# Optimization experiments

Hardware: AMD Instinct MI355X
Metric: run time of the kernel (lower is better)

## Reference

```python
import jax, jax.numpy as jnp
import numpy as np

B, S, D, H, L, E, F, K, V = 4, 1024, 768, 12, 2, 8, 3072, 2, 50257
HD = D // H
EPS = 1e-6
N_TIME, N_LOC, N_ROAD, N_WEATHER = 288, 1000, 10, 8


def rmsnorm(x, w):
    return x / jnp.sqrt(jnp.mean(x * x, axis=-1, keepdims=True) + EPS) * w


def rope_cache(seq_len, dim):
    inv_freq = 1.0 / (10000.0 ** (jnp.arange(0, dim, 2, dtype=jnp.float32) / dim))
    freqs = jnp.arange(seq_len, dtype=jnp.float32)[:, None] * inv_freq[None, :]
    emb = jnp.concatenate([freqs, freqs], axis=-1)  # [S, HD]
    return jnp.cos(emb), jnp.sin(emb)


def rotate_half(x):
    h = x.shape[-1] // 2
    return jnp.concatenate([-x[..., h:], x[..., :h]], axis=-1)


def attention(x, Wq, Wk, Wv, Wo, cos, sin):
    b, s, d = x.shape
    def heads(w):
        return (x @ w).reshape(b, s, H, HD).transpose(0, 2, 1, 3)  # [B,H,S,HD]
    q, k, v = heads(Wq), heads(Wk), heads(Wv)
    c, sn = cos[None, None], sin[None, None]
    q = q * c + rotate_half(q) * sn
    k = k * c + rotate_half(k) * sn
    scores = jnp.einsum('bhqd,bhkd->bhqk', q, k) / jnp.sqrt(jnp.float32(HD))
    mask = jnp.tril(jnp.ones((s, s), dtype=bool))
    scores = jnp.where(mask[None, None], scores, jnp.finfo(scores.dtype).min)
    probs = jax.nn.softmax(scores, axis=-1)
    out = jnp.einsum('bhqk,bhkd->bhqd', probs, v)
    return out.transpose(0, 2, 1, 3).reshape(b, s, d) @ Wo


def moe(x, router_w, Wg, Wu, Wd):
    # x: [T, D]; top-k routed SwiGLU experts, combine weights renormalized over top-k
    probs = jax.nn.softmax(x @ router_w, axis=-1)              # [T, E]
    w, idx = jax.lax.top_k(probs, K)                           # [T, K]
    w = w / jnp.sum(w, axis=-1, keepdims=True)
    onehot = jax.nn.one_hot(idx, E, dtype=x.dtype)             # [T, K, E]
    combine = jnp.sum(onehot * w[..., None], axis=1)           # [T, E]
    out = jnp.zeros_like(x)
    for e in range(E):  # small fixed expert count
        h = jax.nn.silu(x @ Wg[e]) * (x @ Wu[e])               # [T, F]
        out = out + combine[:, e, None] * (h @ Wd[e])
    usage = jnp.mean(jnp.sum(onehot, axis=1), axis=0)          # [E]
    aux = jnp.sum(usage * jnp.mean(probs, axis=0)) * E
    return out, aux


def setup_inputs() -> dict:
    key = jax.random.key(0)
    ks = jax.random.split(key, 40)
    p = lambda i, shape: 0.02 * jax.random.normal(ks[i], shape, dtype=jnp.float32)
    inp = {}
    inp['input_ids'] = jax.random.randint(ks[0], (B, S), 0, V)
    inp['time_slots'] = jax.random.randint(ks[1], (B, 1), 0, N_TIME)
    inp['day_of_week'] = jax.random.randint(ks[2], (B, 1), 0, 7)
    inp['month'] = jax.random.randint(ks[3], (B, 1), 0, 12)
    inp['is_holiday'] = jax.random.randint(ks[4], (B, 1), 0, 2)
    inp['location_ids'] = jax.random.randint(ks[5], (B, 1), 0, N_LOC)
    inp['road_types'] = jax.random.randint(ks[6], (B, 1), 0, N_ROAD)
    inp['weather_states'] = jax.random.randint(ks[7], (B, 1), 0, N_WEATHER)
    inp['word_emb'] = p(8, (V, D))
    inp['time_emb'] = p(9, (N_TIME, D // 4))
    inp['dow_emb'] = p(10, (7, D // 4))
    inp['month_emb'] = p(11, (12, D // 4))
    inp['hol_emb'] = p(12, (2, D // 4))
    inp['loc_emb'] = p(13, (N_LOC, D // 2))
    inp['road_emb'] = p(14, (N_ROAD, D // 4))
    inp['weather_emb'] = p(15, (N_WEATHER, D // 4))
    inp['proj_w'] = p(16, (3 * D, D))
    inp['proj_b'] = jnp.zeros((D,), dtype=jnp.float32)
    inp['emb_norm_w'] = jnp.ones((D,), dtype=jnp.float32)
    inp['norm1_w'] = jnp.ones((L, D), dtype=jnp.float32)
    inp['Wq'] = p(17, (L, D, D))
    inp['Wk'] = p(18, (L, D, D))
    inp['Wv'] = p(19, (L, D, D))
    inp['Wo'] = p(20, (L, D, D))
    inp['norm2_w'] = jnp.ones((L, D), dtype=jnp.float32)
    inp['router_w'] = p(21, (L, D, E))
    inp['Wg'] = p(22, (L, E, D, F))
    inp['Wu'] = p(23, (L, E, D, F))
    inp['Wd'] = p(24, (L, E, F, D))
    inp['final_norm_w'] = jnp.ones((D,), dtype=jnp.float32)
    return inp


def reference(input_ids, time_slots, day_of_week, month, is_holiday, location_ids,
              road_types, weather_states, word_emb, time_emb, dow_emb, month_emb,
              hol_emb, loc_emb, road_emb, weather_emb, proj_w, proj_b, emb_norm_w,
              norm1_w, Wq, Wk, Wv, Wo, norm2_w, router_w, Wg, Wu, Wd, final_norm_w):
    b, s = input_ids.shape
    we = word_emb[input_ids]                                                  # [B,S,D]
    te = jnp.concatenate([time_emb[time_slots], dow_emb[day_of_week],
                          month_emb[month], hol_emb[is_holiday]], axis=-1)    # [B,1,D]
    le = loc_emb[location_ids]                                                # [B,1,D/2]
    ce = jnp.concatenate([road_emb[road_types], weather_emb[weather_states]], axis=-1)
    te = jnp.broadcast_to(te, (b, s, D))
    le = jnp.broadcast_to(le, (b, s, D // 2))
    ce = jnp.broadcast_to(ce, (b, s, D // 2))
    x = jnp.concatenate([we, te, le, ce], axis=-1) @ proj_w + proj_b          # [B,S,D]
    x = rmsnorm(x, emb_norm_w)
    cos, sin = rope_cache(s, HD)
    aux_total = jnp.float32(0.0)
    for l in range(L):
        x = x + attention(rmsnorm(x, norm1_w[l]), Wq[l], Wk[l], Wv[l], Wo[l], cos, sin)
        m, aux = moe(rmsnorm(x, norm2_w[l]).reshape(b * s, D),
                     router_w[l], Wg[l], Wu[l], Wd[l])
        x = x + m.reshape(b, s, D)
        aux_total = aux_total + aux
    x = rmsnorm(x, final_norm_w)
    return x, aux_total
```

## Files before the change

kernel.cpp:

```cpp
#include <hip/hip_runtime.h>
#include <math.h>


#define TTOK 4096
#define FDIM 3072
#define MAXSLOT 9216

typedef __attribute__((ext_vector_type(8))) short short8;
typedef __attribute__((ext_vector_type(4))) float f32x4;

__device__ __forceinline__ float bf2f(unsigned short u) {
  return __uint_as_float(((unsigned int)u) << 16);
}
__device__ __forceinline__ unsigned short f2bf(float f) {
  unsigned int u = __float_as_uint(f);
  u += 0x7fffu + ((u >> 16) & 1u);
  return (unsigned short)(u >> 16);
}
__device__ __forceinline__ void split3f(float a, unsigned short& h, unsigned short& m,
                                        unsigned short& l) {
  h = f2bf(a);
  float r = a - bf2f(h);
  m = f2bf(r);
  r -= bf2f(m);
// ... 76 lines not shown
    dst[di] = h; dst[di + dPS] = m; dst[di + 2 * dPS] = lo;
  }
}

__global__ void tconv2_k(const float* __restrict__ src, unsigned short* __restrict__ dst,
                         size_t dPS, int K, int N, size_t sstride, size_t dstride) {
  __shared__ float tile[32][33];
  src += (size_t)blockIdx.z * sstride;
  size_t dbase = (size_t)blockIdx.z * dstride;
  int n0 = blockIdx.x * 32, k0 = blockIdx.y * 32;
  int tx = threadIdx.x, ty = threadIdx.y;
  #pragma unroll
  for (int r = 0; r < 4; ++r)
    tile[ty + r * 8][tx] = src[(size_t)(k0 + ty + r * 8) * N + n0 + tx];
  __syncthreads();
  #pragma unroll
  for (int r = 0; r < 4; ++r) {
    int n = n0 + ty + r * 8;
    unsigned short h, m;
    split2f(tile[tx][ty + r * 8], h, m);
    size_t di = dbase + (size_t)n * K + k0 + tx;
    dst[di] = h; dst[di + dPS] = m;
  }
}

__global__ void tconv_k(const float* __restrict__ src, unsigned short* __restrict__ dst,
                        int K, int N, size_t sstride, size_t dstride) {
  __shared__ unsigned short tile[32][33];
  src += (size_t)blockIdx.z * sstride;
  unsigned short* d = dst + (size_t)blockIdx.z * dstride;
  int n0 = blockIdx.x * 32, k0 = blockIdx.y * 32;
  int tx = threadIdx.x, ty = threadIdx.y;
  #pragma unroll
  for (int r = 0; r < 4; ++r)
    tile[ty + r * 8][tx] = f2bf(src[(size_t)(k0 + ty + r * 8) * N + n0 + tx]);
  __syncthreads();
  #pragma unroll
  for (int r = 0; r < 4; ++r) {
    int n = n0 + ty + r * 8;
    d[(size_t)n * K + k0 + tx] = tile[tx][ty + r * 8];
  }
}

__global__ void gconv3_k(const float* __restrict__ we, const int* __restrict__ ids,
                         unsigned short* __restrict__ x3, size_t pPS) {
  int t = blockIdx.x;
  int d = threadIdx.x << 2;
  float4 v = *(const float4*)(we + (size_t)ids[t] * 768 + d);
  ushort4 vh, vm, vl;
  split3f(v.x, vh.x, vm.x, vl.x);
  split3f(v.y, vh.y, vm.y, vl.y);
  split3f(v.z, vh.z, vm.z, vl.z);
  split3f(v.w, vh.w, vm.w, vl.w);
  size_t o = (size_t)t * 768 + d;
  *(ushort4*)(x3 + o) = vh;
  *(ushort4*)(x3 + pPS + o) = vm;
  *(ushort4*)(x3 + 2 * pPS + o) = vl;
}

template <int OUT>
__global__ __launch_bounds__(256) void rmsnorm_k(const float* __restrict__ xin,
                                                 const float* __restrict__ w,
                                                 float* __restrict__ yf,
                                                 unsigned short* __restrict__ yb, size_t pPS) {
  int t = blockIdx.x;
  int tid = threadIdx.x;
  const float* xr = xin + (size_t)t * 768;
  float v0 = xr[tid], v1 = xr[tid + 256], v2 = xr[tid + 512];
  float ss = v0 * v0 + v1 * v1 + v2 * v2;
  #pragma unroll
  for (int o = 32; o > 0; o >>= 1) ss += __shfl_xor(ss, o);
  __shared__ float wss[4];
  if ((tid & 63) == 0) wss[tid >> 6] = ss;
  __syncthreads();
  float tot = wss[0] + wss[1] + wss[2] + wss[3];
  float inv = 1.0f / sqrtf(tot / 768.0f + 1e-6f);
  float o0 = v0 * inv * w[tid], o1 = v1 * inv * w[tid + 256], o2 = v2 * inv * w[tid + 512];
  if (OUT != 1) {
    float* yr = yf + (size_t)t * 768;
    yr[tid] = o0; yr[tid + 256] = o1; yr[tid + 512] = o2;
  }
  if (OUT == 1 || OUT == 2) {
    unsigned short* yr = yb + (size_t)t * 768;
    unsigned short h, m, l;
    split3f(o0, h, m, l); yr[tid] = h;       yr[tid + pPS] = m;       yr[tid + 2 * pPS] = l;
    split3f(o1, h, m, l); yr[tid + 256] = h; yr[tid + 256 + pPS] = m; yr[tid + 256 + 2 * pPS] = l;
    split3f(o2, h, m, l); yr[tid + 512] = h; yr[tid + 512 + pPS] = m; yr[tid + 512 + 2 * pPS] = l;
  }
  if (OUT == 3) {
    unsigned short* yr = yb + (size_t)t * 768;
    yr[tid] = f2bf(o0); yr[tid + 256] = f2bf(o1); yr[tid + 512] = f2bf(o2);
  }
}

__global__ __launch_bounds__(256) void rope_apply_k(float* __restrict__ qkv,
                                                    const float* __restrict__ cosb,
                                                    const float* __restrict__ sinb) {
  int idx = blockIdx.x * 256 + threadIdx.x;
  int j = idx & 31;
  int hh = (idx >> 5) % 12;
  int t = idx / 384;
  int s = t & 1023;
  float c = cosb[s * 32 + j], sn = sinb[s * 32 + j];
  size_t base = (size_t)t * 2304 + hh * 64 + j;
  float q1 = qkv[base], q2 = qkv[base + 32];
  qkv[base]      = q1 * c - q2 * sn;
  qkv[base + 32] = q2 * c + q1 * sn;
  size_t kb = base + 768;
  float k1 = qkv[kb], k2 = qkv[kb + 32];
  qkv[kb]      = k1 * c - k2 * sn;
  qkv[kb + 32] = k2 * c + k1 * sn;
}

template <int EPI>
__global__ __launch_bounds__(256) void gemm3(const unsigned short* __restrict__ A, size_t aPS,
                                             const unsigned short* __restrict__ BT, size_t bPS,
                                             float* __restrict__ Cf, int N, int K,
                                             const float* __restrict__ rowBias) {
  __shared__ __align__(16) unsigned short As[3][4096];
  __shared__ __align__(16) unsigned short Bs[3][4096];
  int tid = threadIdx.x, w = tid >> 6, l = tid & 63, lr = l & 15, lg = l >> 4;
  int m0 = blockIdx.y * 128, n0 = blockIdx.x * 128;
  size_t aoff = (size_t)(m0 + 32 * w + lr) * K + lg * 8;
  size_t boff = (size_t)(n0 + 32 * w + lr) * K + lg * 8;
  size_t aoff1 = aoff + (size_t)16 * K, boff1 = boff + (size_t)16 * K;
  f32x4 acc[4][4];
  #pragma unroll
  for (int i = 0; i < 4; ++i)
    #pragma unroll
    for (int j = 0; j < 4; ++j) acc[i][j] = (f32x4){0.f, 0.f, 0.f, 0.f};
  int wr = w >> 1, wc = w & 1;
  for (int k0 = 0; k0 < K; k0 += 32) {
    #pragma unroll
    for (int p = 0; p < 3; ++p) {
      gload16(A + p * aPS + aoff + k0,  &As[p][1024 * w]);
      gload16(A + p * aPS + aoff1 + k0, &As[p][1024 * w + 512]);
      gload16(BT + p * bPS + boff + k0,  &Bs[p][1024 * w]);
      gload16(BT + p * bPS + boff1 + k0, &Bs[p][1024 * w + 512]);
    }
    __syncthreads();
    short8 af[3][4], bf[3][4];
    #pragma unroll
    for (int p = 0; p < 3; ++p)
      #pragma unroll
      for (int i = 0; i < 4; ++i) {
        af[p][i] = *(const short8*)(&As[p][(wr * 4 + i) * 512 + l * 8]);
        bf[p][i] = *(const short8*)(&Bs[p][(wc * 4 + i) * 512 + l * 8]);
      }
    MFMA_SPLIT3(acc)
    __syncthreads();
  }
  int colb = n0 + wc * 64 + lr;
  int rowb = m0 + wr * 64 + lg * 4;
  #pragma unroll
  for (int i = 0; i < 4; ++i)
    #pragma unroll
    for (int j = 0; j < 4; ++j) {
      int col = colb + j * 16;
      #pragma unroll
      for (int r = 0; r < 4; ++r) {
        int row = rowb + i * 16 + r;
        size_t idx = (size_t)row * N + col;
        float v = acc[i][j][r];
        if (EPI == 0)      Cf[idx] = v;
        else if (EPI == 2) Cf[idx] += v;
        else               Cf[idx] = v + rowBias[(row >> 10) * 768 + col];
      }
    }
}

template <int FUSE>
__global__ __launch_bounds__(256) void gemm2_gu(const unsigned short* __restrict__ X3, size_t xPS,
    const unsigned short* __restrict__ W2, size_t wPS, float* __restrict__ outb,
    const float* __restrict__ gin, const int* __restrict__ slot_token,
    const int* __restrict__ offs, const unsigned short* __restrict__ zp) {
  __shared__ __align__(16) unsigned short As[2][4096];
  __shared__ __align__(16) unsigned short Bs[2][4096];
  int sb = blockIdx.y * 128;
  if (sb >= offs[8]) return;
  int e = 0;
  #pragma unroll
  for (int i = 1; i < 8; ++i) if (sb >= offs[i]) e = i;
  int tid = threadIdx.x, w = tid >> 6, l = tid & 63, lr = l & 15, lg = l >> 4;
  int n0 = blockIdx.x * 128;
  const unsigned short* WE = W2 + (size_t)e * FDIM * 768;
  int t0 = slot_token[sb + 32 * w + lr];
  int t1 = slot_token[sb + 32 * w + 16 + lr];
  const unsigned short* a0[2];
  const unsigned short* a1[2];
  #pragma unroll
  for (int p = 0; p < 2; ++p) {
    a0[p] = (t0 < 0 ? zp : X3 + p * xPS + (size_t)t0 * 768) + lg * 8;
    a1[p] = (t1 < 0 ? zp : X3 + p * xPS + (size_t)t1 * 768) + lg * 8;
  }
  size_t boff = (size_t)(n0 + 32 * w + lr) * 768 + lg * 8;
  size_t boff1 = boff + (size_t)16 * 768;
  f32x4 acc[4][4];
  #pragma unroll
  for (int i = 0; i < 4; ++i)
    #pragma unroll
    for (int j = 0; j < 4; ++j) acc[i][j] = (f32x4){0.f, 0.f, 0.f, 0.f};
  int wr = w >> 1, wc = w & 1;
  for (int k0 = 0; k0 < 768; k0 += 32) {
    #pragma unroll
    for (int p = 0; p < 2; ++p) {
      gload16(a0[p] + k0, &As[p][1024 * w]);
      gload16(a1[p] + k0, &As[p][1024 * w + 512]);
      gload16(WE + p * wPS + boff + k0,  &Bs[p][1024 * w]);
      gload16(WE + p * wPS + boff1 + k0, &Bs[p][1024 * w + 512]);
    }
    __syncthreads();
    short8 af[2][4], bf[2][4];
    #pragma unroll
    for (int p = 0; p < 2; ++p)
      #pragma unroll
      for (int i = 0; i < 4; ++i) {
        af[p][i] = *(const short8*)(&As[p][(wr * 4 + i) * 512 + l * 8]);
        bf[p][i] = *(const short8*)(&Bs[p][(wc * 4 + i) * 512 + l * 8]);
      }
    MFMA_SPLIT2(acc)
    __syncthreads();
  }
  int colb = n0 + wc * 64 + lr;
  int rowb = sb + wr * 64 + lg * 4;
  #pragma unroll
  for (int i = 0; i < 4; ++i)
    #pragma unroll
    for (int j = 0; j < 4; ++j) {
      int col = colb + j * 16;
      #pragma unroll
      for (int r = 0; r < 4; ++r) {
        size_t idx = (size_t)(rowb + i * 16 + r) * FDIM + col;
        float v = acc[i][j][r];
        if (FUSE == 0) outb[idx] = v;
        else {
          float g = gin[idx];
          outb[idx] = g / (1.0f + expf(-g)) * v;
        }
      }
    }
}

__global__ __launch_bounds__(256) void gemm2_dn(const float* __restrict__ hbf,
    const unsigned short* __restrict__ W2, size_t wPS, float* __restrict__ ob,
    const int* __restrict__ offs) {
  __shared__ __align__(16) unsigned short As[2][4096];
  __shared__ __align__(16) unsigned short Bs[2][4096];
  int sb = blockIdx.y * 128;
  if (sb >= offs[8]) return;
  int e = 0;
  #pragma unroll
  for (int i = 1; i < 8; ++i) if (sb >= offs[i]) e = i;
  int tid = threadIdx.x, w = tid >> 6, l = tid & 63, lr = l & 15, lg = l >> 4;
  int n0 = blockIdx.x * 128;
  const unsigned short* WE = W2 + (size_t)e * 768 * FDIM;
  size_t boff = (size_t)(n0 + 32 * w + lr) * FDIM + lg * 8;
  size_t boff1 = boff + (size_t)16 * FDIM;
  const float* ha0 = hbf + (size_t)(sb + 32 * w + lr) * FDIM + lg * 8;
  const float* ha1 = ha0 + (size_t)16 * FDIM;
  f32x4 acc[4][4];
  #pragma unroll
  for (int i = 0; i < 4; ++i)
    #pragma unroll
    for (int j = 0; j < 4; ++j) acc[i][j] = (f32x4){0.f, 0.f, 0.f, 0.f};
  int wr = w >> 1, wc = w & 1;
  for (int k0 = 0; k0 < FDIM; k0 += 32) {
    #pragma unroll
    for (int p = 0; p < 2; ++p) {
      gload16(WE + p * wPS + boff + k0,  &Bs[p][1024 * w]);
      gload16(WE + p * wPS + boff1 + k0, &Bs[p][1024 * w + 512]);
    }
    {
      float4 v0 = *(const float4*)(ha0 + k0);
      float4 v1 = *(const float4*)(ha0 + k0 + 4);
      float va[8] = {v0.x, v0.y, v0.z, v0.w, v1.x, v1.y, v1.z, v1.w};
      short8 sh, sm;
      #pragma unroll
      for (int q = 0; q < 8; ++q) {
        unsigned short a, b;
        split2f(va[q], a, b);
        sh[q] = (short)a; sm[q] = (short)b;
      }
      *(short8*)(&As[0][1024 * w + l * 8]) = sh;
      *(short8*)(&As[1][1024 * w + l * 8]) = sm;
      v0 = *(const float4*)(ha1 + k0);
      v1 = *(const float4*)(ha1 + k0 + 4);
      float vb[8] = {v0.x, v0.y, v0.z, v0.w, v1.x, v1.y, v1.z, v1.w};
      #pragma unroll
      for (int q = 0; q < 8; ++q) {
        unsigned short a, b;
        split2f(vb[q], a, b);
        sh[q] = (short)a; sm[q] = (short)b;
      }
      *(short8*)(&As[0][1024 * w + 512 + l * 8]) = sh;
      *(short8*)(&As[1][1024 * w + 512 + l * 8]) = sm;
    }
    __syncthreads();
    short8 af[2][4], bf[2][4];
    #pragma unroll
    for (int p = 0; p < 2; ++p)
      #pragma unroll
      for (int i = 0; i < 4; ++i) {
        af[p][i] = *(const short8*)(&As[p][(wr * 4 + i) * 512 + l * 8]);
        bf[p][i] = *(const short8*)(&Bs[p][(wc * 4 + i) * 512 + l * 8]);
      }
    MFMA_SPLIT2(acc)
    __syncthreads();
  }
  int colb = n0 + wc * 64 + lr;
  int rowb = sb + wr * 64 + lg * 4;
  #pragma unroll
  for (int i = 0; i < 4; ++i)
    #pragma unroll
    for (int j = 0; j < 4; ++j) {
      int col = colb + j * 16;
      #pragma unroll
      for (int r = 0; r < 4; ++r)
        ob[(size_t)(rowb + i * 16 + r) * 768 + col] = acc[i][j][r];
    }
}


__global__ __launch_bounds__(256) void gemm_gu(const unsigned short* __restrict__ xnb,
    const unsigned short* __restrict__ wgT, const unsigned short* __restrict__ wuT,
    unsigned short* __restrict__ hb, const int* __restrict__ slot_token,
    const int* __restrict__ offs, const unsigned short* __restrict__ zp) {
  __shared__ __align__(16) unsigned short As[4096], Bg[4096], Bu[4096];
  int sb = blockIdx.y * 128;
  if (sb >= offs[8]) return;
  int e = 0;
  #pragma unroll
  for (int i = 1; i < 8; ++i) if (sb >= offs[i]) e = i;
  int tid = threadIdx.x, w = tid >> 6, l = tid & 63, lr = l & 15, lg = l >> 4;
  int n0 = blockIdx.x * 128;
  int t0 = slot_token[sb + 32 * w + lr];
  int t1 = slot_token[sb + 32 * w + 16 + lr];
  const unsigned short* ga0 = (t0 < 0 ? zp : xnb + (size_t)t0 * 768) + lg * 8;
  const unsigned short* ga1 = (t1 < 0 ? zp : xnb + (size_t)t1 * 768) + lg * 8;
  const unsigned short* WgE = wgT + (size_t)e * FDIM * 768;
  const unsigned short* WuE = wuT + (size_t)e * FDIM * 768;
  const unsigned short* gg0 = WgE + (size_t)(n0 + 32 * w + lr) * 768 + lg * 8;
  const unsigned short* gg1 = gg0 + 16 * 768;
  const unsigned short* gu0 = WuE + (size_t)(n0 + 32 * w + lr) * 768 + lg * 8;
  const unsigned short* gu1 = gu0 + 16 * 768;
  f32x4 ag[4][4], au[4][4];
  #pragma unroll
  for (int i = 0; i < 4; ++i)
    #pragma unroll
    for (int j = 0; j < 4; ++j) {
      ag[i][j] = (f32x4){0.f, 0.f, 0.f, 0.f};
      au[i][j] = (f32x4){0.f, 0.f, 0.f, 0.f};
    }
  int wr = w >> 1, wc = w & 1;
  for (int k0 = 0; k0 < 768; k0 += 32) {
    gload16(ga0 + k0, As + 1024 * w);
    gload16(ga1 + k0, As + 1024 * w + 512);
    gload16(gg0 + k0, Bg + 1024 * w);
    gload16(gg1 + k0, Bg + 1024 * w + 512);
    gload16(gu0 + k0, Bu + 1024 * w);
    gload16(gu1 + k0, Bu + 1024 * w + 512);
    __syncthreads();
    short8 af[4];
    #pragma unroll
    for (int i = 0; i < 4; ++i) af[i] = *(const short8*)(As + (wr * 4 + i) * 512 + l * 8);
    #pragma unroll
    for (int j = 0; j < 4; ++j) {
      short8 bg = *(const short8*)(Bg + (wc * 4 + j) * 512 + l * 8);
      short8 bu = *(const short8*)(Bu + (wc * 4 + j) * 512 + l * 8);
      #pragma unroll
      for (int i = 0; i < 4; ++i) {
        ag[i][j] = __builtin_amdgcn_mfma_f32_16x16x32_bf16(af[i], bg, ag[i][j], 0, 0, 0);
        au[i][j] = __builtin_amdgcn_mfma_f32_16x16x32_bf16(af[i], bu, au[i][j], 0, 0, 0);
      }
    }
    __syncthreads();
  }
  int colb = n0 + wc * 64 + lr;
  int rowb = sb + wr * 64 + lg * 4;
  #pragma unroll
  for (int i = 0; i < 4; ++i)
    #pragma unroll
    for (int j = 0; j < 4; ++j) {
      int col = colb + j * 16;
      #pragma unroll
      for (int r = 0; r < 4; ++r) {
        float g = ag[i][j][r], u = au[i][j][r];
        hb[(size_t)(rowb + i * 16 + r) * FDIM + col] = f2bf(g / (1.0f + expf(-g)) * u);
      }
    }
}

__global__ __launch_bounds__(256) void gemm_d(const unsigned short* __restrict__ hb,
    const unsigned short* __restrict__ wdT, unsigned short* __restrict__ ob,
    const int* __restrict__ offs) {
  __shared__ __align__(16) unsigned short As[4096], Bs[4096];
  int sb = blockIdx.y * 128;
  if (sb >= offs[8]) return;
  int e = 0;
  #pragma unroll
  for (int i = 1; i < 8; ++i) if (sb >= offs[i]) e = i;
  int tid = threadIdx.x, w = tid >> 6, l = tid & 63, lr = l & 15, lg = l >> 4;
  int n0 = blockIdx.x * 128;
  const unsigned short* ga0 = hb + (size_t)(sb + 32 * w + lr) * FDIM + lg * 8;
  const unsigned short* ga1 = ga0 + (size_t)16 * FDIM;
  const unsigned short* WdE = wdT + (size_t)e * 768 * FDIM;
  const unsigned short* gb0 = WdE + (size_t)(n0 + 32 * w + lr) * FDIM + lg * 8;
  const unsigned short* gb1 = gb0 + (size_t)16 * FDIM;
  f32x4 acc[4][4];
  #pragma unroll
  for (int i = 0; i < 4; ++i)
    #pragma unroll
    for (int j = 0; j < 4; ++j) acc[i][j] = (f32x4){0.f, 0.f, 0.f, 0.f};
  int wr = w >> 1, wc = w & 1;
  for (int k0 = 0; k0 < FDIM; k0 += 32) {
    gload16(ga0 + k0, As + 1024 * w);
    gload16(ga1 + k0, As + 1024 * w + 512);
    gload16(gb0 + k0, Bs + 1024 * w);
    gload16(gb1 + k0, Bs + 1024 * w + 512);
    __syncthreads();
    short8 af[4], bf[4];
    #pragma unroll
    for (int i = 0; i < 4; ++i) af[i] = *(const short8*)(As + (wr * 4 + i) * 512 + l * 8);
    #pragma unroll
    for (int j = 0; j < 4; ++j) bf[j] = *(const short8*)(Bs + (wc * 4 + j) * 512 + l * 8);
    #pragma unroll
    for (int i = 0; i < 4; ++i)
      #pragma unroll
      for (int j = 0; j < 4; ++j)
        acc[i][j] = __builtin_amdgcn_mfma_f32_16x16x32_bf16(af[i], bf[j], acc[i][j], 0, 0, 0);
    __syncthreads();
  }
  int colb = n0 + wc * 64 + lr;
  int rowb = sb + wr * 64 + lg * 4;
  #pragma unroll
  for (int i = 0; i < 4; ++i)
    #pragma unroll
    for (int j = 0; j < 4; ++j) {
      int col = colb + j * 16;
      #pragma unroll
      for (int r = 0; r < 4; ++r)
        ob[(size_t)(rowb + i * 16 + r) * 768 + col] = f2bf(acc[i][j][r]);
    }
}

__global__ __launch_bounds__(256) void attn_k(const float* __restrict__ qkv,
                                              unsigned short* __restrict__ ax3, size_t pPS) {
  int pr = blockIdx.x, h = blockIdx.y, b = blockIdx.z;
  int tid = threadIdx.x;
  int ty4 = (tid >> 4) << 2, tx4 = (tid & 15) << 2;
  __shared__ float qs[64][68];
  __shared__ float kps[64][68];
  __shared__ float vs[64][68];
  int lr = tid >> 2;
  int lc = (tid & 3) << 4;
  for (int half = 0; half < 2; ++half) {
    int qt = half ? (15 - pr) : pr;
    int q0 = qt << 6;
    size_t qbase = ((size_t)(b * 1024 + q0 + lr)) * 2304 + h * 64 + lc;
    #pragma unroll
    for (int i = 0; i < 4; ++i) {
      float4 v = *(const float4*)(qkv + qbase + 4 * i);
      qs[lc + 4 * i + 0][lr] = v.x;
      qs[lc + 4 * i + 1][lr] = v.y;
      qs[lc + 4 * i + 2][lr] = v.z;
      qs[lc + 4 * i + 3][lr] = v.w;
    }
    float acc[4][4];
    float m[4], l[4];
    #pragma unroll
    for (int i = 0; i < 4; ++i) {
      m[i] = -3.0e38f; l[i] = 0.0f;
      #pragma unroll
      for (int j = 0; j < 4; ++j) acc[i][j] = 0.0f;
    }
    for (int kt = 0; kt <= qt; ++kt) {
      int k0 = kt << 6;
      __syncthreads();
      size_t kb = ((size_t)(b * 1024 + k0 + lr)) * 2304 + 768 + h * 64 + lc;
      #pragma unroll
      for (int i = 0; i < 4; ++i) {
        float4 kv = *(const float4*)(qkv + kb + 4 * i);
        kps[lc + 4 * i + 0][lr] = kv.x;
        kps[lc + 4 * i + 1][lr] = kv.y;
        kps[lc + 4 * i + 2][lr] = kv.z;
        kps[lc + 4 * i + 3][lr] = kv.w;
        *(float4*)&vs[lr][lc + 4 * i] = *(const float4*)(qkv + kb + 768 + 4 * i);
      }
      __syncthreads();
      float s[4][4];
      #pragma unroll
      for (int i = 0; i < 4; ++i)
        #pragma unroll
        for (int j = 0; j < 4; ++j) s[i][j] = 0.0f;
      #pragma unroll 8
      for (int d = 0; d < 64; ++d) {
        float4 qv = *(const float4*)&qs[d][ty4];
        float4 kv = *(const float4*)&kps[d][tx4];
        float qa[4] = {qv.x, qv.y, qv.z, qv.w};
        float ka[4] = {kv.x, kv.y, kv.z, kv.w};
        #pragma unroll
        for (int i = 0; i < 4; ++i)
          #pragma unroll
          for (int j = 0; j < 4; ++j) s[i][j] += qa[i] * ka[j];
      }
      bool diag = (kt == qt);
      #pragma unroll
      for (int i = 0; i < 4; ++i) {
        #pragma unroll
        for (int j = 0; j < 4; ++j) {
          if (diag && (tx4 + j > ty4 + i)) s[i][j] = -1.0e30f;
          else s[i][j] *= 0.125f;
        }
        float mx = fmaxf(fmaxf(s[i][0], s[i][1]), fmaxf(s[i][2], s[i][3]));
        mx = fmaxf(mx, __shfl_xor(mx, 1));
        mx = fmaxf(mx, __shfl_xor(mx, 2));
        mx = fmaxf(mx, __shfl_xor(mx, 4));
        mx = fmaxf(mx, __shfl_xor(mx, 8));
        float mnew = fmaxf(m[i], mx);
        float c = expf(m[i] - mnew);
        float rs = 0.0f;
        #pragma unroll
        for (int j = 0; j < 4; ++j) { s[i][j] = expf(s[i][j] - mnew); rs += s[i][j]; }
        rs += __shfl_xor(rs, 1);
        rs += __shfl_xor(rs, 2);
        rs += __shfl_xor(rs, 4);
        rs += __shfl_xor(rs, 8);
        l[i] = l[i] * c + rs;
        m[i] = mnew;
        #pragma unroll
        for (int j = 0; j < 4; ++j) acc[i][j] *= c;
      }
      __syncthreads();
      #pragma unroll
      for (int i = 0; i < 4; ++i)
        *(float4*)&kps[ty4 + i][tx4] = make_float4(s[i][0], s[i][1], s[i][2], s[i][3]);
      __syncthreads();
      #pragma unroll 4
      for (int kk = 0; kk < 16; ++kk) {
        float4 v0 = *(const float4*)&vs[(kk << 2) + 0][tx4];
        float4 v1 = *(const float4*)&vs[(kk << 2) + 1][tx4];
        float4 v2 = *(const float4*)&vs[(kk << 2) + 2][tx4];
        float4 v3 = *(const float4*)&vs[(kk << 2) + 3][tx4];
        #pragma unroll
        for (int i = 0; i < 4; ++i) {
          float4 p4 = *(const float4*)&kps[ty4 + i][kk << 2];
          acc[i][0] += p4.x * v0.x + p4.y * v1.x + p4.z * v2.x + p4.w * v3.x;
          acc[i][1] += p4.x * v0.y + p4.y * v1.y + p4.z * v2.y + p4.w * v3.y;
          acc[i][2] += p4.x * v0.z + p4.y * v1.z + p4.z * v2.z + p4.w * v3.z;
          acc[i][3] += p4.x * v0.w + p4.y * v1.w + p4.z * v2.w + p4.w * v3.w;
        }
      }
    }
    __syncthreads();
    #pragma unroll
    for (int i = 0; i < 4; ++i) {
      float invl = 1.0f / l[i];
      size_t ob = ((size_t)(b * 1024 + q0 + ty4 + i)) * 768 + h * 64 + tx4;
      ushort4 vh, vm, vl;
      unsigned short a0, a1, a2;
      split3f(acc[i][0] * invl, a0, a1, a2); vh.x = a0; vm.x = a1; vl.x = a2;
      split3f(acc[i][1] * invl, a0, a1, a2); vh.y = a0; vm.y = a1; vl.y = a2;
      split3f(acc[i][2] * invl, a0, a1, a2); vh.z = a0; vm.z = a1; vl.z = a2;
      split3f(acc[i][3] * invl, a0, a1, a2); vh.w = a0; vm.w = a1; vl.w = a2;
      *(ushort4*)(ax3 + ob) = vh;
      *(ushort4*)(ax3 + pPS + ob) = vm;
      *(ushort4*)(ax3 + 2 * pPS + ob) = vl;
    }
  }
}

__global__ __launch_bounds__(256) void router_k(const float* __restrict__ xn,
                                                const float* __restrict__ rw,
                                                int* __restrict__ tk_idx, float* __restrict__ tk_w,
                                                int* __restrict__ cnt, float* __restrict__ psum) {
  __shared__ float bps[8];
  __shared__ int bcnt[8];
  int tid = threadIdx.x;
  if (tid < 8) { bps[tid] = 0.0f; bcnt[tid] = 0; }
  __syncthreads();
  int t = blockIdx.x * 4 + (tid >> 6);
  int lane = tid & 63;
  const float* xr = xn + (size_t)t * 768;
  float p[8] = {};
  for (int d = lane; d < 768; d += 64) {
    float xv = xr[d];
    const float* wr = rw + (size_t)d * 8;
    #pragma unroll
    for (int e = 0; e < 8; ++e) p[e] += xv * wr[e];
  }
  #pragma unroll
  for (int e = 0; e < 8; ++e) {
    float v = p[e];
    #pragma unroll
    for (int o = 32; o > 0; o >>= 1) v += __shfl_xor(v, o);
    p[e] = v;
  }
  if (lane == 0) {
    float mx = p[0];
    #pragma unroll
    for (int e = 1; e < 8; ++e) mx = fmaxf(mx, p[e]);
    float s = 0.0f;
    #pragma unroll
    for (int e = 0; e < 8; ++e) { p[e] = expf(p[e] - mx); s += p[e]; }
    float invs = 1.0f / s;
    #pragma unroll
    for (int e = 0; e < 8; ++e) p[e] *= invs;
    int i1 = 0; float v1 = p[0];
    #pragma unroll
    for (int e = 1; e < 8; ++e) if (p[e] > v1) { v1 = p[e]; i1 = e; }
    int i2 = (i1 == 0) ? 1 : 0; float v2 = p[i2];
    #pragma unroll
    for (int e = 0; e < 8; ++e) if (e != i1 && p[e] > v2) { v2 = p[e]; i2 = e; }
    float wsum = v1 + v2;
    tk_idx[t * 2] = i1; tk_idx[t * 2 + 1] = i2;
    tk_w[t * 2] = v1 / wsum; tk_w[t * 2 + 1] = v2 / wsum;
    atomicAdd(&bcnt[i1], 1); atomicAdd(&bcnt[i2], 1);
    #pragma unroll
    for (int e = 0; e < 8; ++e) atomicAdd(&bps[e], p[e]);
  }
  __syncthreads();
  if (tid < 8) {
    atomicAdd(&cnt[tid], bcnt[tid]);
    atomicAdd(&psum[tid], bps[tid]);
  }
}

__global__ void moe_offsets_k(const int* __restrict__ cnt, int* __restrict__ offs,
                              const float* __restrict__ psum, float* __restrict__ aux) {
  if (threadIdx.x == 0) {
    int o = 0; float a = 0.0f;
    for (int e = 0; e < 8; ++e) {
      offs[e] = o;
      o += (cnt[e] + 127) & ~127;
      a += ((float)cnt[e] / 4096.0f) * (psum[e] / 4096.0f);
    }
    offs[8] = o;
    aux[0] += a * 8.0f;
  }
}

__global__ void moe_fill_k(const int* __restrict__ tk_idx, const int* __restrict__ offs,
                           int* __restrict__ fill, int* __restrict__ slot_token,
                           int* __restrict__ tk_slot) {
  int i = blockIdx.x * 256 + threadIdx.x;
  int e = tk_idx[i];
  int pos = atomicAdd(&fill[e], 1);
  int slot = offs[e] + pos;
  slot_token[slot] = i >> 1;
  tk_slot[i] = slot;
}

template <int BF>
__global__ void moe_combine_k(float* __restrict__ x, const void* __restrict__ osv,
                              const int* __restrict__ tk_slot, const float* __restrict__ tk_w) {
  int t = blockIdx.x;
  int d = threadIdx.x << 2;
  int s0 = tk_slot[t * 2], s1 = tk_slot[t * 2 + 1];
  float w0 = tk_w[t * 2], w1 = tk_w[t * 2 + 1];
  float a0, a1, a2, a3, b0, b1, b2, b3;
  if (BF == 0) {
    const float* os = (const float*)osv;
    float4 a = *(const float4*)(os + (size_t)s0 * 768 + d);
    float4 b = *(const float4*)(os + (size_t)s1 * 768 + d);
    a0 = a.x; a1 = a.y; a2 = a.z; a3 = a.w;
    b0 = b.x; b1 = b.y; b2 = b.z; b3 = b.w;
  } else {
    const unsigned short* os = (const unsigned short*)osv;
    ushort4 a = *(const ushort4*)(os + (size_t)s0 * 768 + d);
    ushort4 b = *(const ushort4*)(os + (size_t)s1 * 768 + d);
    a0 = bf2f(a.x); a1 = bf2f(a.y); a2 = bf2f(a.z); a3 = bf2f(a.w);
    b0 = bf2f(b.x); b1 = bf2f(b.y); b2 = bf2f(b.z); b3 = bf2f(b.w);
  }
  float4 c = *(const float4*)(x + (size_t)t * 768 + d);
  c.x += w0 * a0 + w1 * b0;
  c.y += w0 * a1 + w1 * b1;
  c.z += w0 * a2 + w1 * b2;
  c.w += w0 * a3 + w1 * b3;
  *(float4*)(x + (size_t)t * 768 + d) = c;
}

__global__ void write_aux_k(const float* __restrict__ aux, float* __restrict__ out) {
  out[0] = aux[0];
}


extern "C" void kernel_launch(void* const* d_in, const int* in_sizes, int n_in,
                              void* d_out, int out_size, void* d_ws, size_t ws_size,
                              hipStream_t stream) {
  const int* input_ids      = (const int*)d_in[0];
  const int* time_slots     = (const int*)d_in[1];
  const int* day_of_week    = (const int*)d_in[2];
  const int* month          = (const int*)d_in[3];
  const int* is_holiday     = (const int*)d_in[4];
  const int* location_ids   = (const int*)d_in[5];
  const int* road_types     = (const int*)d_in[6];
  const int* weather_states = (const int*)d_in[7];
  const float* word_emb     = (const float*)d_in[8];
  const float* time_emb     = (const float*)d_in[9];
  const float* dow_emb      = (const float*)d_in[10];
  const float* month_emb    = (const float*)d_in[11];
  const float* hol_emb      = (const float*)d_in[12];
  const float* loc_emb      = (const float*)d_in[13];
  const float* road_emb     = (const float*)d_in[14];
  const float* weather_emb  = (const float*)d_in[15];
  const float* proj_w       = (const float*)d_in[16];
  const float* proj_b       = (const float*)d_in[17];
  const float* emb_norm_w   = (const float*)d_in[18];
  const float* norm1_w     = (const float*)d_in[19];
  const float* Wq           = (const float*)d_in[20];
  const float* Wk           = (const float*)d_in[21];
  const float* Wv           = (const float*)d_in[22];
  const float* Wo           = (const float*)d_in[23];
  const float* norm2_w      = (const float*)d_in[24];
  const float* router_w     = (const float*)d_in[25];
  const float* Wg           = (const float*)d_in[26];
  const float* Wu           = (const float*)d_in[27];
  const float* Wd           = (const float*)d_in[28];
  const float* final_norm_w = (const float*)d_in[29];
  float* out = (float*)d_out;

  const size_t TD = (size_t)TTOK * 768;
  const size_t REG = (size_t)MAXSLOT * FDIM * 4;
  char* base = (char*)d_ws;
  auto carve = [&](size_t bytes) { char* p = base; base += (bytes + 255) & ~(size_t)255; return p; };
  float* x    = (float*)carve(TD * 4);
  float* xn   = (float*)carve(TD * 4);
  float* cosb = (float*)carve(32768 * 4);
  float* sinb = (float*)carve(32768 * 4);
  float* ctx  = (float*)carve(4 * 1536 * 4);
  float* biasB= (float*)carve(4 * 768 * 4);
  float* tkw  = (float*)carve(8192 * 4);
  float* psum = (float*)carve(64);
  float* auxa = (float*)carve(64);
  int* cnt    = (int*)carve(64);
  int* fill   = (int*)carve(64);
  int* offs   = (int*)carve(64);
  int* tk_idx = (int*)carve(8192 * 4);
  int* tk_slot= (int*)carve(8192 * 4);
  int* slot_token = (int*)carve(MAXSLOT * 4);
  unsigned short* zp = (unsigned short*)carve(4096);
  unsigned short* xnb3 = (unsigned short*)carve(3 * TD * 2);
  char* QAH = carve(REG);
  char* GT  = carve(REG);
  char* Wr  = carve(REG);
  float* qkv = (float*)QAH;
  unsigned short* ax3 = (unsigned short*)(QAH + (size_t)TTOK * 2304 * 4);
  float* hbf = (float*)QAH;
  unsigned short* hb16 = (unsigned short*)QAH;
  float* gtmp = (float*)GT;
  float* obf = (float*)GT;
  unsigned short* ob16 = (unsigned short*)GT;
  unsigned short* wpl = (unsigned short*)Wr;

  const size_t PS_D = (size_t)768 * 768;
  const size_t PS_QKV = (size_t)2304 * 768;
  const size_t PS_E = (size_t)8 * FDIM * 768;

  hipMemsetAsync(auxa, 0, 64, stream);
  hipMemsetAsync(zp, 0, 4096, stream);
  rope_cache_k<<<dim3(1024), dim3(32), 0, stream>>>(cosb, sinb);
  build_ctx_k<<<dim3(4, 6), dim3(256), 0, stream>>>(time_slots, day_of_week, month, is_holiday,
      location_ids, road_types, weather_states, time_emb, dow_emb, month_emb, hol_emb,
      loc_emb, road_emb, weather_emb, ctx);
  build_bias_k<<<dim3(4, 3), dim3(256), 0, stream>>>(ctx, proj_w, proj_b, biasB);
  tconv3_k<<<dim3(24, 24, 1), dim3(32, 8), 0, stream>>>(proj_w, wpl, PS_D, 768, 768, 0, 0);
  gconv3_k<<<dim3(TTOK), dim3(192), 0, stream>>>(word_emb, input_ids, xnb3, TD);
  gemm3<3><<<dim3(6, 32), dim3(256), 0, stream>>>(xnb3, TD, wpl, PS_D, xn, 768, 768, biasB);
  rmsnorm_k<0><<<dim3(TTOK), dim3(256), 0, stream>>>(xn, emb_norm_w, x, nullptr, 0);

  for (int l = 0; l < 2; ++l) {
    const float* rw = router_w + (size_t)l * 768 * 8;
    tconv3_k<<<dim3(24, 24, 1), dim3(32, 8), 0, stream>>>(Wq + (size_t)l * PS_D, wpl, PS_QKV, 768, 768, 0, 0);
    tconv3_k<<<dim3(24, 24, 1), dim3(32, 8), 0, stream>>>(Wk + (size_t)l * PS_D, wpl + PS_D, PS_QKV, 768, 768, 0, 0);
    tconv3_k<<<dim3(24, 24, 1), dim3(32, 8), 0, stream>>>(Wv + (size_t)l * PS_D, wpl + 2 * PS_D, PS_QKV, 768, 768, 0, 0);
    rmsnorm_k<1><<<dim3(TTOK), dim3(256), 0, stream>>>(x, norm1_w + l * 768, nullptr, xnb3, TD);
    gemm3<0><<<dim3(18, 32), dim3(256), 0, stream>>>(xnb3, TD, wpl, PS_QKV, qkv, 2304, 768, nullptr);
    rope_apply_k<<<dim3(6144), dim3(256), 0, stream>>>(qkv, cosb, sinb);
    attn_k<<<dim3(8, 12, 4), dim3(256), 0, stream>>>(qkv, ax3, TD);
    tconv3_k<<<dim3(24, 24, 1), dim3(32, 8), 0, stream>>>(Wo + (size_t)l * PS_D, wpl, PS_D, 768, 768, 0, 0);
    gemm3<2><<<dim3(6, 32), dim3(256), 0, stream>>>(ax3, TD, wpl, PS_D, x, 768, 768, nullptr);

    if (l == 0)
      rmsnorm_k<2><<<dim3(TTOK), dim3(256), 0, stream>>>(x, norm2_w, xn, xnb3, TD);
    else
      rmsnorm_k<3><<<dim3(TTOK), dim3(256), 0, stream>>>(x, norm2_w + 768, xn, xnb3, TD);
    hipMemsetAsync(cnt, 0, 64, stream);
    hipMemsetAsync(fill, 0, 64, stream);
    hipMemsetAsync(psum, 0, 64, stream);
    hipMemsetAsync(slot_token, 0xFF, MAXSLOT * 4, stream);
    router_k<<<dim3(1024), dim3(256), 0, stream>>>(xn, rw, tk_idx, tkw, cnt, psum);
    moe_offsets_k<<<dim3(1), dim3(64), 0, stream>>>(cnt, offs, psum, auxa);
    moe_fill_k<<<dim3(32), dim3(256), 0, stream>>>(tk_idx, offs, fill, slot_token, tk_slot);
    if (l == 0) {
      tconv2_k<<<dim3(96, 24, 8), dim3(32, 8), 0, stream>>>(Wg, wpl, PS_E,
          768, FDIM, (size_t)768 * FDIM, (size_t)FDIM * 768);
      gemm2_gu<0><<<dim3(24, MAXSLOT / 128), dim3(256), 0, stream>>>(xnb3, TD, wpl, PS_E,
          gtmp, nullptr, slot_token, offs, zp);
      tconv2_k<<<dim3(96, 24, 8), dim3(32, 8), 0, stream>>>(Wu, wpl, PS_E,
          768, FDIM, (size_t)768 * FDIM, (size_t)FDIM * 768);
      gemm2_gu<1><<<dim3(24, MAXSLOT / 128), dim3(256), 0, stream>>>(xnb3, TD, wpl, PS_E,
          hbf, gtmp, slot_token, offs, zp);
      tconv2_k<<<dim3(24, 96, 8), dim3(32, 8), 0, stream>>>(Wd, wpl, PS_E,
          FDIM, 768, (size_t)FDIM * 768, (size_t)768 * FDIM);
      gemm2_dn<<<dim3(6, MAXSLOT / 128), dim3(256), 0, stream>>>(hbf, wpl, PS_E, obf, offs);
      moe_combine_k<0><<<dim3(TTOK), dim3(192), 0, stream>>>(x, obf, tk_slot, tkw);
    } else {
      const float* wg1 = Wg + (size_t)8 * 768 * FDIM;
      const float* wu1 = Wu + (size_t)8 * 768 * FDIM;
      const float* wd1 = Wd + (size_t)8 * FDIM * 768;
      tconv_k<<<dim3(96, 24, 8), dim3(32, 8), 0, stream>>>(wg1, wpl,
          768, FDIM, (size_t)768 * FDIM, (size_t)FDIM * 768);
      tconv_k<<<dim3(96, 24, 8), dim3(32, 8), 0, stream>>>(wu1, wpl + PS_E,
          768, FDIM, (size_t)768 * FDIM, (size_t)FDIM * 768);
      gemm_gu<<<dim3(24, MAXSLOT / 128), dim3(256), 0, stream>>>(xnb3, wpl, wpl + PS_E,
          hb16, slot_token, offs, zp);
      tconv_k<<<dim3(24, 96, 8), dim3(32, 8), 0, stream>>>(wd1, wpl,
          FDIM, 768, (size_t)FDIM * 768, (size_t)768 * FDIM);
      gemm_d<<<dim3(6, MAXSLOT / 128), dim3(256), 0, stream>>>(hb16, wpl, ob16, offs);
      moe_combine_k<1><<<dim3(TTOK), dim3(192), 0, stream>>>(x, ob16, tk_slot, tkw);
    }
  }

  rmsnorm_k<0><<<dim3(TTOK), dim3(256), 0, stream>>>(x, final_norm_w, out, nullptr, 0);
  write_aux_k<<<dim3(1), dim3(1), 0, stream>>>(auxa, out + TD);
}
```

Baseline: 2.323 ms.

## Use two-way bf16 splits for attention GEMMs and split layer-1 gate/up GEMM

The QKV and output-projection GEMMs now take two-term bf16 splits (hi+mid) instead of three-term ones, through a new gemm2 kernel, with matching changes in rmsnorm, attention output and weight conversion. This cuts MFMA work and memory traffic for those projections but lowers their precision. Separately, the layer-1 fused gate/up GEMM is split into a kernel with twice the column blocks that writes gate and up as bf16, followed by a separate SiLU-multiply pass. That lowers register pressure per block at the cost of an extra round trip through memory for the intermediate.

New measurement: 2.129 ms. 1.09x faster.

```diff
diff --git a/kernel.cpp b/kernel.cpp
--- a/kernel.cpp
+++ b/kernel.cpp
@@ -182,10 +182,10 @@
   }
   if (OUT == 1 || OUT == 2) {
     unsigned short* yr = yb + (size_t)t * 768;
-    unsigned short h, m, l;
-    split3f(o0, h, m, l); yr[tid] = h;       yr[tid + pPS] = m;       yr[tid + 2 * pPS] = l;
-    split3f(o1, h, m, l); yr[tid + 256] = h; yr[tid + 256 + pPS] = m; yr[tid + 256 + 2 * pPS] = l;
-    split3f(o2, h, m, l); yr[tid + 512] = h; yr[tid + 512 + pPS] = m; yr[tid + 512 + 2 * pPS] = l;
+    unsigned short h, m;
+    split2f(o0, h, m); yr[tid] = h;       yr[tid + pPS] = m;
+    split2f(o1, h, m); yr[tid + 256] = h; yr[tid + 256 + pPS] = m;
+    split2f(o2, h, m); yr[tid + 512] = h; yr[tid + 512 + pPS] = m;
   }
   if (OUT == 3) {
     unsigned short* yr = yb + (size_t)t * 768;
@@ -269,6 +269,61 @@
     }
 }
 
+template <int EPI>
+__global__ __launch_bounds__(256) void gemm2(const unsigned short* __restrict__ A, size_t aPS,
+                                             const unsigned short* __restrict__ BT, size_t bPS,
+                                             float* __restrict__ Cf, int N, int K) {
+  __shared__ __align__(16) unsigned short As[2][4096];
+  __shared__ __align__(16) unsigned short Bs[2][4096];
+  int tid = threadIdx.x, w = tid >> 6, l = tid & 63, lr = l & 15, lg = l >> 4;
+  int m0 = blockIdx.y * 128, n0 = blockIdx.x * 128;
+  size_t aoff = (size_t)(m0 + 32 * w + lr) * K + lg * 8;
+  size_t boff = (size_t)(n0 + 32 * w + lr) * K + lg * 8;
+  size_t aoff1 = aoff + (size_t)16 * K, boff1 = boff + (size_t)16 * K;
+  f32x4 acc[4][4];
+  #pragma unroll
+  for (int i = 0; i < 4; ++i)
+    #pragma unroll
+    for (int j = 0; j < 4; ++j) acc[i][j] = (f32x4){0.f, 0.f, 0.f, 0.f};
+  int wr = w >> 1, wc = w & 1;
+  for (int k0 = 0; k0 < K; k0 += 32) {
+    #pragma unroll
+    for (int p = 0; p < 2; ++p) {
+      gload16(A + p * aPS + aoff + k0,  &As[p][1024 * w]);
+      gload16(A + p * aPS + aoff1 + k0, &As[p][1024 * w + 512]);
+      gload16(BT + p * bPS + boff + k0,  &Bs[p][1024 * w]);
+      gload16(BT + p * bPS + boff1 + k0, &Bs[p][1024 * w + 512]);
+    }
+    __syncthreads();
+    short8 af[2][4], bf[2][4];
+    #pragma unroll
+    for (int p = 0; p < 2; ++p)
+      #pragma unroll
+      for (int i = 0; i < 4; ++i) {
+        af[p][i] = *(const short8*)(&As[p][(wr * 4 + i) * 512 + l * 8]);
+        bf[p][i] = *(const short8*)(&Bs[p][(wc * 4 + i) * 512 + l * 8]);
+      }
+    MFMA_SPLIT2(acc)
+    __syncthreads();
+  }
+  int colb = n0 + wc * 64 + lr;
+  int rowb = m0 + wr * 64 + lg * 4;
+  #pragma unroll
+  for (int i = 0; i < 4; ++i)
+    #pragma unroll
+    for (int j = 0; j < 4; ++j) {
+      int col = colb + j * 16;
+      #pragma unroll
+      for (int r = 0; r < 4; ++r) {
+        int row = rowb + i * 16 + r;
+        size_t idx = (size_t)row * N + col;
+        float v = acc[i][j][r];
+        if (EPI == 0) Cf[idx] = v;
+        else          Cf[idx] += v;
+      }
+    }
+}
+
 template <int FUSE>
 __global__ __launch_bounds__(256) void gemm2_gu(const unsigned short* __restrict__ X3, size_t xPS,
     const unsigned short* __restrict__ W2, size_t wPS, float* __restrict__ outb,
@@ -420,12 +475,11 @@
     }
 }
 
-
-__global__ __launch_bounds__(256) void gemm_gu(const unsigned short* __restrict__ xnb,
+__global__ __launch_bounds__(256) void gemm_gu2(const unsigned short* __restrict__ xnb,
     const unsigned short* __restrict__ wgT, const unsigned short* __restrict__ wuT,
-    unsigned short* __restrict__ hb, const int* __restrict__ slot_token,
+    unsigned short* __restrict__ gub, const int* __restrict__ slot_token,
     const int* __restrict__ offs, const unsigned short* __restrict__ zp) {
-  __shared__ __align__(16) unsigned short As[4096], Bg[4096], Bu[4096];
+  __shared__ __align__(16) unsigned short As[4096], Bs[4096];
   int sb = blockIdx.y * 128;
   if (sb >= offs[8]) return;
   int e = 0;
@@ -433,49 +487,40 @@
   for (int i = 1; i < 8; ++i) if (sb >= offs[i]) e = i;
   int tid = threadIdx.x, w = tid >> 6, l = tid & 63, lr = l & 15, lg = l >> 4;
   int n0 = blockIdx.x * 128;
+  int nl = (n0 < FDIM) ? n0 : (n0 - FDIM);
+  const unsigned short* WE = ((n0 < FDIM) ? wgT : wuT) + (size_t)e * FDIM * 768;
+  unsigned short* OB = (n0 < FDIM) ? gub : (gub + (size_t)MAXSLOT * FDIM);
   int t0 = slot_token[sb + 32 * w + lr];
   int t1 = slot_token[sb + 32 * w + 16 + lr];
   const unsigned short* ga0 = (t0 < 0 ? zp : xnb + (size_t)t0 * 768) + lg * 8;
   const unsigned short* ga1 = (t1 < 0 ? zp : xnb + (size_t)t1 * 768) + lg * 8;
-  const unsigned short* WgE = wgT + (size_t)e * FDIM * 768;
-  const unsigned short* WuE = wuT + (size_t)e * FDIM * 768;
-  const unsigned short* gg0 = WgE + (size_t)(n0 + 32 * w + lr) * 768 + lg * 8;
-  const unsigned short* gg1 = gg0 + 16 * 768;
-  const unsigned short* gu0 = WuE + (size_t)(n0 + 32 * w + lr) * 768 + lg * 8;
-  const unsigned short* gu1 = gu0 + 16 * 768;
-  f32x4 ag[4][4], au[4][4];
-  #pragma unroll
-  for (int i = 0; i < 4; ++i)
-    #pragma unroll
-    for (int j = 0; j < 4; ++j) {
-      ag[i][j] = (f32x4){0.f, 0.f, 0.f, 0.f};
-      au[i][j] = (f32x4){0.f, 0.f, 0.f, 0.f};
-    }
+  const unsigned short* gb0 = WE + (size_t)(nl + 32 * w + lr) * 768 + lg * 8;
+  const unsigned short* gb1 = gb0 + 16 * 768;
+  f32x4 acc[4][4];
+  #pragma unroll
+  for (int i = 0; i < 4; ++i)
+    #pragma unroll
+    for (int j = 0; j < 4; ++j) acc[i][j] = (f32x4){0.f, 0.f, 0.f, 0.f};
   int wr = w >> 1, wc = w & 1;
   for (int k0 = 0; k0 < 768; k0 += 32) {
     gload16(ga0 + k0, As + 1024 * w);
     gload16(ga1 + k0, As + 1024 * w + 512);
-    gload16(gg0 + k0, Bg + 1024 * w);
-    gload16(gg1 + k0, Bg + 1024 * w + 512);
-    gload16(gu0 + k0, Bu + 1024 * w);
-    gload16(gu1 + k0, Bu + 1024 * w + 512);
-    __syncthreads();
-    short8 af[4];
+    gload16(gb0 + k0, Bs + 1024 * w);
+    gload16(gb1 + k0, Bs + 1024 * w + 512);
+    __syncthreads();
+    short8 af[4], bf[4];
     #pragma unroll
     for (int i = 0; i < 4; ++i) af[i] = *(const short8*)(As + (wr * 4 + i) * 512 + l * 8);
     #pragma unroll
-    for (int j = 0; j < 4; ++j) {
-      short8 bg = *(const short8*)(Bg + (wc * 4 + j) * 512 + l * 8);
-      short8 bu = *(const short8*)(Bu + (wc * 4 + j) * 512 + l * 8);
-      #pragma unroll
-      for (int i = 0; i < 4; ++i) {
-        ag[i][j] = __builtin_amdgcn_mfma_f32_16x16x32_bf16(af[i], bg, ag[i][j], 0, 0, 0);
-        au[i][j] = __builtin_amdgcn_mfma_f32_16x16x32_bf16(af[i], bu, au[i][j], 0, 0, 0);
-      }
-    }
-    __syncthreads();
-  }
-  int colb = n0 + wc * 64 + lr;
+    for (int j = 0; j < 4; ++j) bf[j] = *(const short8*)(Bs + (wc * 4 + j) * 512 + l * 8);
+    #pragma unroll
+    for (int i = 0; i < 4; ++i)
+      #pragma unroll
+      for (int j = 0; j < 4; ++j)
+        acc[i][j] = __builtin_amdgcn_mfma_f32_16x16x32_bf16(af[i], bf[j], acc[i][j], 0, 0, 0);
+    __syncthreads();
+  }
+  int colb = nl + wc * 64 + lr;
   int rowb = sb + wr * 64 + lg * 4;
   #pragma unroll
   for (int i = 0; i < 4; ++i)
@@ -483,11 +528,34 @@
     for (int j = 0; j < 4; ++j) {
       int col = colb + j * 16;
       #pragma unroll
-      for (int r = 0; r < 4; ++r) {
-        float g = ag[i][j][r], u = au[i][j][r];
-        hb[(size_t)(rowb + i * 16 + r) * FDIM + col] = f2bf(g / (1.0f + expf(-g)) * u);
-      }
-    }
+      for (int r = 0; r < 4; ++r)
+        OB[(size_t)(rowb + i * 16 + r) * FDIM + col] = f2bf(acc[i][j][r]);
+    }
+}
+
+__global__ void silu_mul_k(const unsigned short* __restrict__ gub,
+                           unsigned short* __restrict__ hb) {
+  size_t i = ((size_t)blockIdx.x * 256 + threadIdx.x) * 8;
+  const unsigned short* u = gub + (size_t)MAXSLOT * FDIM;
+  ushort4 g0 = *(const ushort4*)(gub + i);
+  ushort4 g1 = *(const ushort4*)(gub + i + 4);
+  ushort4 u0 = *(const ushort4*)(u + i);
+  ushort4 u1 = *(const ushort4*)(u + i + 4);
+  float gf[8] = {bf2f(g0.x), bf2f(g0.y), bf2f(g0.z), bf2f(g0.w),
+                 bf2f(g1.x), bf2f(g1.y), bf2f(g1.z), bf2f(g1.w)};
+  float uf[8] = {bf2f(u0.x), bf2f(u0.y), bf2f(u0.z), bf2f(u0.w),
+                 bf2f(u1.x), bf2f(u1.y), bf2f(u1.z), bf2f(u1.w)};
+  ushort4 h0, h1;
+  h0.x = f2bf(gf[0] / (1.0f + expf(-gf[0])) * uf[0]);
+  h0.y = f2bf(gf[1] / (1.0f + expf(-gf[1])) * uf[1]);
+  h0.z = f2bf(gf[2] / (1.0f + expf(-gf[2])) * uf[2]);
+  h0.w = f2bf(gf[3] / (1.0f + expf(-gf[3])) * uf[3]);
+  h1.x = f2bf(gf[4] / (1.0f + expf(-gf[4])) * uf[4]);
+  h1.y = f2bf(gf[5] / (1.0f + expf(-gf[5])) * uf[5]);
+  h1.z = f2bf(gf[6] / (1.0f + expf(-gf[6])) * uf[6]);
+  h1.w = f2bf(gf[7] / (1.0f + expf(-gf[7])) * uf[7]);
+  *(ushort4*)(hb + i) = h0;
+  *(ushort4*)(hb + i + 4) = h1;
 }
 
 __global__ __launch_bounds__(256) void gemm_d(const unsigned short* __restrict__ hb,
@@ -544,7 +612,7 @@
 }
 
 __global__ __launch_bounds__(256) void attn_k(const float* __restrict__ qkv,
-                                              unsigned short* __restrict__ ax3, size_t pPS) {
+                                              unsigned short* __restrict__ ax2, size_t pPS) {
   int pr = blockIdx.x, h = blockIdx.y, b = blockIdx.z;
   int tid = threadIdx.x;
   int ty4 = (tid >> 4) << 2, tx4 = (tid & 15) << 2;
@@ -656,15 +724,14 @@
     for (int i = 0; i < 4; ++i) {
       float invl = 1.0f / l[i];
       size_t ob = ((size_t)(b * 1024 + q0 + ty4 + i)) * 768 + h * 64 + tx4;
-      ushort4 vh, vm, vl;
-      unsigned short a0, a1, a2;
-      split3f(acc[i][0] * invl, a0, a1, a2); vh.x = a0; vm.x = a1; vl.x = a2;
-      split3f(acc[i][1] * invl, a0, a1, a2); vh.y = a0; vm.y = a1; vl.y = a2;
-      split3f(acc[i][2] * invl, a0, a1, a2); vh.z = a0; vm.z = a1; vl.z = a2;
-      split3f(acc[i][3] * invl, a0, a1, a2); vh.w = a0; vm.w = a1; vl.w = a2;
-      *(ushort4*)(ax3 + ob) = vh;
-      *(ushort4*)(ax3 + pPS + ob) = vm;
-      *(ushort4*)(ax3 + 2 * pPS + ob) = vl;
+      ushort4 vh, vm;
+      unsigned short a0, a1;
+      split2f(acc[i][0] * invl, a0, a1); vh.x = a0; vm.x = a1;
+      split2f(acc[i][1] * invl, a0, a1); vh.y = a0; vm.y = a1;
+      split2f(acc[i][2] * invl, a0, a1); vh.z = a0; vm.z = a1;
+      split2f(acc[i][3] * invl, a0, a1); vh.w = a0; vm.w = a1;
+      *(ushort4*)(ax2 + ob) = vh;
+      *(ushort4*)(ax2 + pPS + ob) = vm;
     }
   }
 }
@@ -806,7 +873,7 @@
   const float* proj_w       = (const float*)d_in[16];
   const float* proj_b       = (const float*)d_in[17];
   const float* emb_norm_w   = (const float*)d_in[18];
-  const float* norm1_w     = (const float*)d_in[19];
+  const float* norm1_w      = (const float*)d_in[19];
   const float* Wq           = (const float*)d_in[20];
   const float* Wk           = (const float*)d_in[21];
   const float* Wv           = (const float*)d_in[22];
@@ -844,11 +911,12 @@
   char* GT  = carve(REG);
   char* Wr  = carve(REG);
   float* qkv = (float*)QAH;
-  unsigned short* ax3 = (unsigned short*)(QAH + (size_t)TTOK * 2304 * 4);
+  unsigned short* ax2 = (unsigned short*)(QAH + (size_t)TTOK * 2304 * 4);
   float* hbf = (float*)QAH;
   unsigned short* hb16 = (unsigned short*)QAH;
   float* gtmp = (float*)GT;
   float* obf = (float*)GT;
+  unsigned short* gu16 = (unsigned short*)GT;
   unsigned short* ob16 = (unsigned short*)GT;
   unsigned short* wpl = (unsigned short*)Wr;
 
@@ -870,15 +938,15 @@
 
   for (int l = 0; l < 2; ++l) {
     const float* rw = router_w + (size_t)l * 768 * 8;
-    tconv3_k<<<dim3(24, 24, 1), dim3(32, 8), 0, stream>>>(Wq + (size_t)l * PS_D, wpl, PS_QKV, 768, 768, 0, 0);
-    tconv3_k<<<dim3(24, 24, 1), dim3(32, 8), 0, stream>>>(Wk + (size_t)l * PS_D, wpl + PS_D, PS_QKV, 768, 768, 0, 0);
-    tconv3_k<<<dim3(24, 24, 1), dim3(32, 8), 0, stream>>>(Wv + (size_t)l * PS_D, wpl + 2 * PS_D, PS_QKV, 768, 768, 0, 0);
+    tconv2_k<<<dim3(24, 24, 1), dim3(32, 8), 0, stream>>>(Wq + (size_t)l * PS_D, wpl, PS_QKV, 768, 768, 0, 0);
+    tconv2_k<<<dim3(24, 24, 1), dim3(32, 8), 0, stream>>>(Wk + (size_t)l * PS_D, wpl + PS_D, PS_QKV, 768, 768, 0, 0);
+    tconv2_k<<<dim3(24, 24, 1), dim3(32, 8), 0, stream>>>(Wv + (size_t)l * PS_D, wpl + 2 * PS_D, PS_QKV, 768, 768, 0, 0);
     rmsnorm_k<1><<<dim3(TTOK), dim3(256), 0, stream>>>(x, norm1_w + l * 768, nullptr, xnb3, TD);
-    gemm3<0><<<dim3(18, 32), dim3(256), 0, stream>>>(xnb3, TD, wpl, PS_QKV, qkv, 2304, 768, nullptr);
+    gemm2<0><<<dim3(18, 32), dim3(256), 0, stream>>>(xnb3, TD, wpl, PS_QKV, qkv, 2304, 768);
     rope_apply_k<<<dim3(6144), dim3(256), 0, stream>>>(qkv, cosb, sinb);
-    attn_k<<<dim3(8, 12, 4), dim3(256), 0, stream>>>(qkv, ax3, TD);
-    tconv3_k<<<dim3(24, 24, 1), dim3(32, 8), 0, stream>>>(Wo + (size_t)l * PS_D, wpl, PS_D, 768, 768, 0, 0);
-    gemm3<2><<<dim3(6, 32), dim3(256), 0, stream>>>(ax3, TD, wpl, PS_D, x, 768, 768, nullptr);
+    attn_k<<<dim3(8, 12, 4), dim3(256), 0, stream>>>(qkv, ax2, TD);
+    tconv2_k<<<dim3(24, 24, 1), dim3(32, 8), 0, stream>>>(Wo + (size_t)l * PS_D, wpl, PS_D, 768, 768, 0, 0);
+    gemm2<2><<<dim3(6, 32), dim3(256), 0, stream>>>(ax2, TD, wpl, PS_D, x, 768, 768);
 
     if (l == 0)
       rmsnorm_k<2><<<dim3(TTOK), dim3(256), 0, stream>>>(x, norm2_w, xn, xnb3, TD);
@@ -912,8 +980,9 @@
           768, FDIM, (size_t)768 * FDIM, (size_t)FDIM * 768);
       tconv_k<<<dim3(96, 24, 8), dim3(32, 8), 0, stream>>>(wu1, wpl + PS_E,
           768, FDIM, (size_t)768 * FDIM, (size_t)FDIM * 768);
-      gemm_gu<<<dim3(24, MAXSLOT / 128), dim3(256), 0, stream>>>(xnb3, wpl, wpl + PS_E,
-          hb16, slot_token, offs, zp);
+      gemm_gu2<<<dim3(48, MAXSLOT / 128), dim3(256), 0, stream>>>(xnb3, wpl, wpl + PS_E,
+          gu16, slot_token, offs, zp);
+      silu_mul_k<<<dim3((int)((size_t)MAXSLOT * FDIM / 2048)), dim3(256), 0, stream>>>(gu16, hb16);
       tconv_k<<<dim3(24, 96, 8), dim3(32, 8), 0, stream>>>(wd1, wpl,
           FDIM, 768, (size_t)FDIM * 768, (size_t)768 * FDIM);
       gemm_d<<<dim3(6, MAXSLOT / 128), dim3(256), 0, stream>>>(hb16, wpl, ob16, offs);
```
